# Kernel tuning notes

Measured on AMD Instinct MI355X. Metric: run time of the kernel, lower is better.

## Reference

```python
import jax, jax.numpy as jnp
import numpy as np

NUM_HEADS = 12


def setup_inputs() -> dict:
    key = jax.random.key(0)
    k1, k2, k3 = jax.random.split(key, 3)
    B, S, D = 8, 1024, 768
    x = jax.random.normal(k1, (B, S, D), dtype=jnp.float32)
    # Linear weights, torch convention [out_features, in_features], small init
    w_qkv = jax.random.normal(k2, (3 * D, D), dtype=jnp.float32) * 0.02
    b_qkv = jnp.zeros((3 * D,), dtype=jnp.float32)
    w_proj = jax.random.normal(k3, (D, D), dtype=jnp.float32) * 0.02
    b_proj = jnp.zeros((D,), dtype=jnp.float32)
    return {"x": x, "w_qkv": w_qkv, "b_qkv": b_qkv, "w_proj": w_proj, "b_proj": b_proj}


def reference(x, w_qkv, b_qkv, w_proj, b_proj):
    B, S, D = x.shape
    H = NUM_HEADS
    hd = D // H
    qkv = x @ w_qkv.T + b_qkv                      # [B, S, 3D]
    qkv = qkv.reshape(B, S, 3, H, hd).transpose(2, 0, 3, 1, 4)  # [3, B, H, S, hd]
    q, k, v = qkv[0], qkv[1], qkv[2]
    # NOTE: source computes self.scale but never applies it -> unscaled QK^T
    weights = jnp.einsum('bhqd,bhkd->bhqk', q, k)  # [B, H, S, S]
    attn = jax.nn.softmax(weights, axis=-1)        # dropout = 0 (eval)
    out = jnp.einsum('bhqk,bhkd->bhqd', attn, v)   # [B, H, S, hd]
    out = out.transpose(0, 2, 1, 3).reshape(B, S, D)
    return out @ w_proj.T + b_proj
```

## Files before the change

kernel.cpp:

```cpp
#include <hip/hip_runtime.h>


typedef short bf16x8 __attribute__((ext_vector_type(8)));
typedef float f32x4  __attribute__((ext_vector_type(4)));

#define MFMA16(a, b, c) __builtin_amdgcn_mfma_f32_16x16x32_bf16((a), (b), (c), 0, 0, 0)

__device__ __forceinline__ unsigned short f2bf(float f) {
    union { float f; unsigned int u; } v; v.f = f;
    unsigned int u = v.u;
    return (unsigned short)((u + 0x7fffu + ((u >> 16) & 1u)) >> 16);
}

__device__ __forceinline__ unsigned int cvt2(float x, float y) {
#if __has_builtin(__builtin_amdgcn_cvt_pk_bf16_f32)
    auto v = __builtin_amdgcn_cvt_pk_bf16_f32(x, y);
    unsigned int b; __builtin_memcpy(&b, &v, 4); return b;
#else
    return (unsigned int)f2bf(x) | ((unsigned int)f2bf(y) << 16);
#endif
}

__device__ __forceinline__ void gl2lds16(const unsigned short* g, unsigned short* l) {
    __builtin_amdgcn_global_load_lds(
        (const unsigned int __attribute__((address_space(1)))*)g,
        (unsigned int __attribute__((address_space(3)))*)l,
        16, 0, 0);
}

__global__ void cvt_kernel(const float* __restrict__ src,
                           unsigned short* __restrict__ dst, int n4) {
    int i = blockIdx.x * blockDim.x + threadIdx.x;
    if (i >= n4) return;
    float4 v = ((const float4*)src)[i];
    ushort4 o;
    o.x = f2bf(v.x); o.y = f2bf(v.y); o.z = f2bf(v.z); o.w = f2bf(v.w);
    ((ushort4*)dst)[i] = o;
}

__global__ __launch_bounds__(256) void gemm_qkv(
    const unsigned short* __restrict__ A,
    const unsigned short* __restrict__ Bm,
    const float* __restrict__ bias,
    unsigned short* __restrict__ Qo,
    unsigned short* __restrict__ Ko,
    unsigned short* __restrict__ Vto) {
    const int K = 768;
    __shared__ __align__(16) unsigned short smem[8704];
    unsigned short* As = smem;
    unsigned short* Bs = smem + 4096;
    const int tid = threadIdx.x;
    const int wave = tid >> 6, lane = tid & 63;
    const int quad = lane >> 4, l16 = lane & 15;
    const int wm = (wave >> 1) * 64, wn = (wave & 1) * 64;
    const int tileM = blockIdx.x * 128, tileN = blockIdx.y * 128;

    f32x4 zero4 = {0.f, 0.f, 0.f, 0.f};
    f32x4 acc[4][4];
#pragma unroll
    for (int i = 0; i < 4; ++i)
#pragma unroll
        for (int j = 0; j < 4; ++j) acc[i][j] = zero4;

    const unsigned short* Ab = A + (size_t)tileM * K;
    const unsigned short* Bb = Bm + (size_t)tileN * K;

    for (int k0 = 0; k0 < K; k0 += 32) {
#pragma unroll
        for (int i = 0; i < 2; ++i) {
            int s = tid + (i << 8);
            int r = s >> 2, c = s & 3;
            gl2lds16(Ab + (size_t)r * K + k0 + c * 8, As + ((wave << 6) + (i << 8)) * 8);
            gl2lds16(Bb + (size_t)r * K + k0 + c * 8, Bs + ((wave << 6) + (i << 8)) * 8);
        }
        __syncthreads();
        bf16x8 af[4], bfr[4];
#pragma unroll
        for (int t = 0; t < 4; ++t) {
            af[t]  = *(const bf16x8*)(As + (wm + t * 16 + l16) * 32 + quad * 8);
            bfr[t] = *(const bf16x8*)(Bs + (wn + t * 16 + l16) * 32 + quad * 8);
        }
#pragma unroll
        for (int tm = 0; tm < 4; ++tm)
#pragma unroll
            for (int tn = 0; tn < 4; ++tn)
                acc[tm][tn] = MFMA16(af[tm], bfr[tn], acc[tm][tn]);
        __syncthreads();
    }

    const int t = blockIdx.y / 6;
    if (t < 2) {
        const float scale = (t == 0) ? 1.44269504f : 1.0f;
        unsigned short* dst = (t == 0) ? Qo : Ko;
#pragma unroll
        for (int tm = 0; tm < 4; ++tm) {
#pragma unroll
            for (int tn = 0; tn < 4; ++tn) {
                int n = tileN + wn + tn * 16 + l16;
                int rem = n - t * 768;
                int h = rem >> 6, d = rem & 63;
                float bv = bias[n];
#pragma unroll
                for (int r = 0; r < 4; ++r) {
                    int m = tileM + wm + tm * 16 + quad * 4 + r;
                    int b = m >> 10, s = m & 1023;
                    dst[((((size_t)b * 12 + h) << 10) + s) * 64 + d] =
                        f2bf((acc[tm][tn][r] + bv) * scale);
                }
            }
        }
    } else {
        const int b = tileM >> 10, srow = tileM & 1023;
#pragma unroll
        for (int h2 = 0; h2 < 2; ++h2) {
            __syncthreads();
            if ((wn >> 6) == h2) {
#pragma unroll
                for (int tn = 0; tn < 4; ++tn) {
                    int dl = tn * 16 + l16;
                    float bv = bias[tileN + wn + dl];
#pragma unroll
                    for (int tm = 0; tm < 4; ++tm) {
                        int mb = wm + tm * 16 + quad * 4;
                        uint2 pk;
                        pk.x = cvt2(acc[tm][tn][0] + bv, acc[tm][tn][1] + bv);
                        pk.y = cvt2(acc[tm][tn][2] + bv, acc[tm][tn][3] + bv);
                        *(uint2*)(smem + dl * 136 + mb) = pk;
                    }
                }
            }
            __syncthreads();
#pragma unroll
            for (int pass = 0; pass < 4; ++pass) {
                int dl = pass * 16 + (tid >> 4), soff = (tid & 15) * 8;
                bf16x8 row = *(const bf16x8*)(smem + dl * 136 + soff);
                int rem = tileN + h2 * 64 + dl - 1536;
                int h = rem >> 6, d = rem & 63;
                *(bf16x8*)(Vto + (((size_t)b * 12 + h) * 64 + d) * 1024 + srow + soff) = row;
            }
        }
    }
}

__global__ __launch_bounds__(256) void attn_kernel(
    const unsigned short* __restrict__ Q,
    const unsigned short* __restrict__ Kg,
    const unsigned short* __restrict__ Vt,
    unsigned short* __restrict__ O) {
    __shared__ __align__(16) unsigned short Qs[2][128 * 32];
    __shared__ __align__(16) unsigned short Ks[2][64 * 32];
    __shared__ __align__(16) unsigned short Vs[2][64 * 32];
    __shared__ __align__(16) unsigned short Ps[128 * 64];

    const int tid = threadIdx.x;
    const int wave = tid >> 6, lane = tid & 63;
    const int quad = lane >> 4, l16 = lane & 15;
    const int s4 = l16 & 3;
    const int qt = blockIdx.x;
    const int bh = blockIdx.y;
    const int b = bh / 12, h = bh - b * 12;

    const unsigned short* Qb = Q  + ((size_t)bh * 1024 + qt * 128) * 64;
    const unsigned short* Kb = Kg + (size_t)bh * 1024 * 64;
    const unsigned short* Vb = Vt + (size_t)bh * 64 * 1024;

#pragma unroll
    for (int half = 0; half < 2; ++half)
#pragma unroll
        for (int i = 0; i < 2; ++i) {
            int s = tid + (i << 8);
            int r = s >> 2, c = s & 3;
            gl2lds16(Qb + r * 64 + half * 32 + c * 8,
                     Qs[half] + ((wave << 6) + (i << 8)) * 8);
        }

    f32x4 zero4 = {0.f, 0.f, 0.f, 0.f};
    f32x4 oacc[2][4], osum[2];
#pragma unroll
    for (int tm = 0; tm < 2; ++tm) {
        osum[tm] = zero4;
#pragma unroll
        for (int tv = 0; tv < 4; ++tv) oacc[tm][tv] = zero4;
    }
    const short one_bf = (short)0x3F80;
    const bf16x8 onef = {one_bf, one_bf, one_bf, one_bf,
                         one_bf, one_bf, one_bf, one_bf};

    for (int kv0 = 0; kv0 < 1024; kv0 += 64) {
        {
            int r = tid >> 2, c = tid & 3;
#pragma unroll
            for (int half = 0; half < 2; ++half) {
                gl2lds16(Kb + (size_t)(kv0 + r) * 64 + half * 32 + c * 8,
                         Ks[half] + (wave << 6) * 8);
                gl2lds16(Vb + (size_t)r * 1024 + kv0 + half * 32 + c * 8,
                         Vs[half] + (wave << 6) * 8);
            }
        }
        __syncthreads();

        f32x4 st[4][2];
#pragma unroll
        for (int tk = 0; tk < 4; ++tk)
#pragma unroll
            for (int tq = 0; tq < 2; ++tq) st[tk][tq] = zero4;
#pragma unroll
        for (int ks = 0; ks < 2; ++ks) {
            bf16x8 kf[4], qf[2];
#pragma unroll
            for (int tk = 0; tk < 4; ++tk)
                kf[tk] = *(const bf16x8*)(Ks[ks] + (tk * 16 + l16) * 32 + quad * 8);
#pragma unroll
            for (int tq = 0; tq < 2; ++tq)
                qf[tq] = *(const bf16x8*)(Qs[ks] + (wave * 32 + tq * 16 + l16) * 32 + quad * 8);
#pragma unroll
            for (int tk = 0; tk < 4; ++tk)
#pragma unroll
                for (int tq = 0; tq < 2; ++tq)
                    st[tk][tq] = MFMA16(kf[tk], qf[tq], st[tk][tq]);
        }

#pragma unroll
        for (int tq = 0; tq < 2; ++tq) {
            unsigned short* prp = Ps + (wave * 32 + tq * 16 + l16) * 64 + quad * 4;
#pragma unroll
            for (int tk = 0; tk < 4; ++tk) {
                float e0 = __builtin_amdgcn_exp2f(st[tk][tq][0]);
                float e1 = __builtin_amdgcn_exp2f(st[tk][tq][1]);
                float e2 = __builtin_amdgcn_exp2f(st[tk][tq][2]);
                float e3 = __builtin_amdgcn_exp2f(st[tk][tq][3]);
                uint2 pk;
                pk.x = cvt2(e0, e1);
                pk.y = cvt2(e2, e3);
                *(uint2*)(prp + ((tk ^ s4) << 4)) = pk;
            }
        }

#pragma unroll
        for (int ks2 = 0; ks2 < 2; ++ks2) {
            bf16x8 ap[2], bv[4];
            int colswz = ((ks2 << 5) + (quad << 3)) ^ (s4 << 4);
#pragma unroll
            for (int tm = 0; tm < 2; ++tm)
                ap[tm] = *(const bf16x8*)(Ps + (wave * 32 + tm * 16 + l16) * 64 + colswz);
#pragma unroll
            for (int tv = 0; tv < 4; ++tv)
                bv[tv] = *(const bf16x8*)(Vs[ks2] + (tv * 16 + l16) * 32 + quad * 8);
#pragma unroll
            for (int tm = 0; tm < 2; ++tm) {
#pragma unroll
                for (int tv = 0; tv < 4; ++tv)
                    oacc[tm][tv] = MFMA16(ap[tm], bv[tv], oacc[tm][tv]);
                osum[tm] = MFMA16(ap[tm], onef, osum[tm]);
            }
        }
        __syncthreads();
    }

#pragma unroll
    for (int tm = 0; tm < 2; ++tm) {
        f32x4 inv;
#pragma unroll
        for (int r = 0; r < 4; ++r) inv[r] = 1.0f / osum[tm][r];
#pragma unroll
        for (int tv = 0; tv < 4; ++tv)
#pragma unroll
            for (int r = 0; r < 4; ++r) {
                int srow = qt * 128 + wave * 32 + tm * 16 + quad * 4 + r;
                int col = h * 64 + tv * 16 + l16;
                O[((size_t)b * 1024 + srow) * 768 + col] = f2bf(oacc[tm][tv][r] * inv[r]);
            }
    }
}

__global__ __launch_bounds__(256) void gemm_proj(
    const unsigned short* __restrict__ A,
    const unsigned short* __restrict__ Bm,
    const float* __restrict__ bias,
    float* __restrict__ out) {
    const int K = 768;
    __shared__ __align__(16) unsigned short As[128 * 32];
    __shared__ __align__(16) unsigned short Bs[128 * 32];
    const int tid = threadIdx.x;
    const int wave = tid >> 6, lane = tid & 63;
    const int quad = lane >> 4, l16 = lane & 15;
    const int wm = (wave >> 1) * 64, wn = (wave & 1) * 64;
    const int tileM = blockIdx.x * 128, tileN = blockIdx.y * 128;

    f32x4 zero4 = {0.f, 0.f, 0.f, 0.f};
    f32x4 acc[4][4];
#pragma unroll
    for (int i = 0; i < 4; ++i)
#pragma unroll
        for (int j = 0; j < 4; ++j) acc[i][j] = zero4;

    const unsigned short* Ab = A + (size_t)tileM * K;
    const unsigned short* Bb = Bm + (size_t)tileN * K;

    for (int k0 = 0; k0 < K; k0 += 32) {
#pragma unroll
        for (int i = 0; i < 2; ++i) {
            int s = tid + (i << 8);
            int r = s >> 2, c = s & 3;
            gl2lds16(Ab + (size_t)r * K + k0 + c * 8, As + ((wave << 6) + (i << 8)) * 8);
            gl2lds16(Bb + (size_t)r * K + k0 + c * 8, Bs + ((wave << 6) + (i << 8)) * 8);
        }
        __syncthreads();
        bf16x8 af[4], bfr[4];
#pragma unroll
        for (int t = 0; t < 4; ++t) {
            af[t]  = *(const bf16x8*)(As + (wm + t * 16 + l16) * 32 + quad * 8);
            bfr[t] = *(const bf16x8*)(Bs + (wn + t * 16 + l16) * 32 + quad * 8);
        }
#pragma unroll
        for (int tm = 0; tm < 4; ++tm)
#pragma unroll
            for (int tn = 0; tn < 4; ++tn)
                acc[tm][tn] = MFMA16(af[tm], bfr[tn], acc[tm][tn]);
        __syncthreads();
    }

#pragma unroll
    for (int tm = 0; tm < 4; ++tm) {
#pragma unroll
        for (int tn = 0; tn < 4; ++tn) {
            int n = tileN + wn + tn * 16 + l16;
            float bv = bias[n];
#pragma unroll
            for (int r = 0; r < 4; ++r) {
                int m = tileM + wm + tm * 16 + quad * 4 + r;
                out[(size_t)m * 768 + n] = acc[tm][tn][r] + bv;
            }
        }
    }
}

extern "C" void kernel_launch(void* const* d_in, const int* in_sizes, int n_in,
                              void* d_out, int out_size, void* d_ws, size_t ws_size,
                              hipStream_t stream) {
    (void)in_sizes; (void)n_in; (void)out_size; (void)ws_size;
    const float* x      = (const float*)d_in[0];
    const float* w_qkv  = (const float*)d_in[1];
    const float* b_qkv  = (const float*)d_in[2];
    const float* w_proj = (const float*)d_in[3];
    const float* b_proj = (const float*)d_in[4];
    float* out = (float*)d_out;

    char* ws = (char*)d_ws;
    unsigned short* xb     = (unsigned short*)(ws + 0);
    unsigned short* wqkvb  = (unsigned short*)(ws + 12582912);
    unsigned short* wprojb = (unsigned short*)(ws + 16121856);
    unsigned short* Qw     = (unsigned short*)(ws + 17301504);
    unsigned short* Kw     = (unsigned short*)(ws + 29884416);
    unsigned short* Vtw    = (unsigned short*)(ws + 42467328);

    cvt_kernel<<<(1572864 + 255) / 256, 256, 0, stream>>>(x, xb, 1572864);
    cvt_kernel<<<(442368 + 255) / 256, 256, 0, stream>>>(w_qkv, wqkvb, 442368);
    cvt_kernel<<<(147456 + 255) / 256, 256, 0, stream>>>(w_proj, wprojb, 147456);

    gemm_qkv<<<dim3(64, 18), 256, 0, stream>>>(xb, wqkvb, b_qkv, Qw, Kw, Vtw);
    attn_kernel<<<dim3(8, 96), 256, 0, stream>>>(Qw, Kw, Vtw, xb);
    gemm_proj<<<dim3(64, 6), 256, 0, stream>>>(xb, wprojb, b_proj, out);
}
```

Baseline: 210.3 us.

## Merge conversion kernels, deepen GEMM K-step, restructure attention Q/K layout and row sums

Merges the three fp32-to-bf16 conversion launches into one kernel. Doubles the K step per barrier in both GEMMs, loading two 32-wide slabs per iteration to halve synchronisation. Q and K are now written in a row-major [B,S,D] layout with coalesced stores instead of per-head scattered stores. The attention kernel keeps Q fragments in registers, accumulates softmax row sums with scalar adds and shuffles instead of an extra MFMA against ones, and aliases its LDS buffers. The trade-offs are more LDS per block, which may reduce occupancy, and strided per-head K/Q loads in attention.

```diff
diff --git a/kernel.cpp b/kernel.cpp
--- a/kernel.cpp
+++ b/kernel.cpp
@@ -28,14 +28,21 @@
         16, 0, 0);
 }
 
-__global__ void cvt_kernel(const float* __restrict__ src,
-                           unsigned short* __restrict__ dst, int n4) {
-    int i = blockIdx.x * blockDim.x + threadIdx.x;
-    if (i >= n4) return;
-    float4 v = ((const float4*)src)[i];
+__global__ void cvt3_kernel(const float* __restrict__ x,
+                            const float* __restrict__ wq,
+                            const float* __restrict__ wp,
+                            unsigned short* __restrict__ xb,
+                            unsigned short* __restrict__ wqb,
+                            unsigned short* __restrict__ wpb) {
+    int i = blockIdx.x * 256 + threadIdx.x;
+    const float* s; unsigned short* d; int off;
+    if (i < 1572864)      { s = x;  d = xb;  off = i; }
+    else if (i < 2015232) { s = wq; d = wqb; off = i - 1572864; }
+    else                  { s = wp; d = wpb; off = i - 2015232; }
+    float4 v = ((const float4*)s)[off];
     ushort4 o;
     o.x = f2bf(v.x); o.y = f2bf(v.y); o.z = f2bf(v.z); o.w = f2bf(v.w);
-    ((ushort4*)dst)[i] = o;
+    ((ushort4*)d)[off] = o;
 }
 
 __global__ __launch_bounds__(256) void gemm_qkv(
@@ -46,9 +53,9 @@
     unsigned short* __restrict__ Ko,
     unsigned short* __restrict__ Vto) {
     const int K = 768;
-    __shared__ __align__(16) unsigned short smem[8704];
-    unsigned short* As = smem;
-    unsigned short* Bs = smem + 4096;
+    __shared__ __align__(16) unsigned short smem[16384];
+    unsigned short* Asv[2] = { smem, smem + 4096 };
+    unsigned short* Bsv[2] = { smem + 8192, smem + 12288 };
     const int tid = threadIdx.x;
     const int wave = tid >> 6, lane = tid & 63;
     const int quad = lane >> 4, l16 = lane & 15;
@@ -65,26 +72,34 @@
     const unsigned short* Ab = A + (size_t)tileM * K;
     const unsigned short* Bb = Bm + (size_t)tileN * K;
 
-    for (int k0 = 0; k0 < K; k0 += 32) {
+    for (int k0 = 0; k0 < K; k0 += 64) {
 #pragma unroll
         for (int i = 0; i < 2; ++i) {
             int s = tid + (i << 8);
             int r = s >> 2, c = s & 3;
-            gl2lds16(Ab + (size_t)r * K + k0 + c * 8, As + ((wave << 6) + (i << 8)) * 8);
-            gl2lds16(Bb + (size_t)r * K + k0 + c * 8, Bs + ((wave << 6) + (i << 8)) * 8);
-        }
-        __syncthreads();
-        bf16x8 af[4], bfr[4];
-#pragma unroll
-        for (int t = 0; t < 4; ++t) {
-            af[t]  = *(const bf16x8*)(As + (wm + t * 16 + l16) * 32 + quad * 8);
-            bfr[t] = *(const bf16x8*)(Bs + (wn + t * 16 + l16) * 32 + quad * 8);
-        }
-#pragma unroll
-        for (int tm = 0; tm < 4; ++tm)
-#pragma unroll
-            for (int tn = 0; tn < 4; ++tn)
-                acc[tm][tn] = MFMA16(af[tm], bfr[tn], acc[tm][tn]);
+            const unsigned short* ga = Ab + (size_t)r * K + k0 + c * 8;
+            const unsigned short* gb = Bb + (size_t)r * K + k0 + c * 8;
+            int dst = ((wave << 6) + (i << 8)) * 8;
+            gl2lds16(ga,      Asv[0] + dst);
+            gl2lds16(ga + 32, Asv[1] + dst);
+            gl2lds16(gb,      Bsv[0] + dst);
+            gl2lds16(gb + 32, Bsv[1] + dst);
+        }
+        __syncthreads();
+#pragma unroll
+        for (int ks = 0; ks < 2; ++ks) {
+            bf16x8 af[4], bfr[4];
+#pragma unroll
+            for (int t = 0; t < 4; ++t) {
+                af[t]  = *(const bf16x8*)(Asv[ks] + (wm + t * 16 + l16) * 32 + quad * 8);
+                bfr[t] = *(const bf16x8*)(Bsv[ks] + (wn + t * 16 + l16) * 32 + quad * 8);
+            }
+#pragma unroll
+            for (int tm = 0; tm < 4; ++tm)
+#pragma unroll
+                for (int tn = 0; tn < 4; ++tn)
+                    acc[tm][tn] = MFMA16(af[tm], bfr[tn], acc[tm][tn]);
+        }
         __syncthreads();
     }
 
@@ -92,20 +107,17 @@
     if (t < 2) {
         const float scale = (t == 0) ? 1.44269504f : 1.0f;
         unsigned short* dst = (t == 0) ? Qo : Ko;
+        const int nb = tileN - t * 768 + wn;
 #pragma unroll
         for (int tm = 0; tm < 4; ++tm) {
 #pragma unroll
             for (int tn = 0; tn < 4; ++tn) {
-                int n = tileN + wn + tn * 16 + l16;
-                int rem = n - t * 768;
-                int h = rem >> 6, d = rem & 63;
-                float bv = bias[n];
+                int nl = nb + tn * 16 + l16;
+                float bv = bias[tileN + wn + tn * 16 + l16];
 #pragma unroll
                 for (int r = 0; r < 4; ++r) {
                     int m = tileM + wm + tm * 16 + quad * 4 + r;
-                    int b = m >> 10, s = m & 1023;
-                    dst[((((size_t)b * 12 + h) << 10) + s) * 64 + d] =
-                        f2bf((acc[tm][tn][r] + bv) * scale);
+                    dst[(size_t)m * 768 + nl] = f2bf((acc[tm][tn][r] + bv) * scale);
                 }
             }
         }
@@ -147,10 +159,11 @@
     const unsigned short* __restrict__ Kg,
     const unsigned short* __restrict__ Vt,
     unsigned short* __restrict__ O) {
-    __shared__ __align__(16) unsigned short Qs[2][128 * 32];
-    __shared__ __align__(16) unsigned short Ks[2][64 * 32];
-    __shared__ __align__(16) unsigned short Vs[2][64 * 32];
-    __shared__ __align__(16) unsigned short Ps[128 * 64];
+    __shared__ __align__(16) unsigned short smem[16384];
+    unsigned short* Ps  = smem;
+    unsigned short* Qsv[2] = { smem, smem + 4096 };
+    unsigned short* Ksv[2] = { smem + 8192,  smem + 10240 };
+    unsigned short* Vsv[2] = { smem + 12288, smem + 14336 };
 
     const int tid = threadIdx.x;
     const int wave = tid >> 6, lane = tid & 63;
@@ -160,42 +173,46 @@
     const int bh = blockIdx.y;
     const int b = bh / 12, h = bh - b * 12;
 
-    const unsigned short* Qb = Q  + ((size_t)bh * 1024 + qt * 128) * 64;
-    const unsigned short* Kb = Kg + (size_t)bh * 1024 * 64;
+    const unsigned short* Qb = Q  + ((size_t)b * 1024 + qt * 128) * 768 + h * 64;
+    const unsigned short* Kb = Kg + (size_t)b * 1024 * 768 + h * 64;
     const unsigned short* Vb = Vt + (size_t)bh * 64 * 1024;
 
 #pragma unroll
-    for (int half = 0; half < 2; ++half)
-#pragma unroll
-        for (int i = 0; i < 2; ++i) {
-            int s = tid + (i << 8);
-            int r = s >> 2, c = s & 3;
-            gl2lds16(Qb + r * 64 + half * 32 + c * 8,
-                     Qs[half] + ((wave << 6) + (i << 8)) * 8);
-        }
+    for (int i = 0; i < 2; ++i) {
+        int s = tid + (i << 8);
+        int r = s >> 2, c = s & 3;
+        const unsigned short* gq = Qb + (size_t)r * 768 + c * 8;
+        int dst = ((wave << 6) + (i << 8)) * 8;
+        gl2lds16(gq,      Qsv[0] + dst);
+        gl2lds16(gq + 32, Qsv[1] + dst);
+    }
+    __syncthreads();
+    bf16x8 qf[2][2];
+#pragma unroll
+    for (int ks = 0; ks < 2; ++ks)
+#pragma unroll
+        for (int tq = 0; tq < 2; ++tq)
+            qf[ks][tq] = *(const bf16x8*)(Qsv[ks] + (wave * 32 + tq * 16 + l16) * 32 + quad * 8);
+    __syncthreads();
 
     f32x4 zero4 = {0.f, 0.f, 0.f, 0.f};
-    f32x4 oacc[2][4], osum[2];
-#pragma unroll
-    for (int tm = 0; tm < 2; ++tm) {
-        osum[tm] = zero4;
+    f32x4 oacc[2][4];
+    float rsum[2] = {0.f, 0.f};
+#pragma unroll
+    for (int tm = 0; tm < 2; ++tm)
 #pragma unroll
         for (int tv = 0; tv < 4; ++tv) oacc[tm][tv] = zero4;
-    }
-    const short one_bf = (short)0x3F80;
-    const bf16x8 onef = {one_bf, one_bf, one_bf, one_bf,
-                         one_bf, one_bf, one_bf, one_bf};
 
     for (int kv0 = 0; kv0 < 1024; kv0 += 64) {
         {
             int r = tid >> 2, c = tid & 3;
-#pragma unroll
-            for (int half = 0; half < 2; ++half) {
-                gl2lds16(Kb + (size_t)(kv0 + r) * 64 + half * 32 + c * 8,
-                         Ks[half] + (wave << 6) * 8);
-                gl2lds16(Vb + (size_t)r * 1024 + kv0 + half * 32 + c * 8,
-                         Vs[half] + (wave << 6) * 8);
-            }
+            const unsigned short* gk = Kb + (size_t)(kv0 + r) * 768 + c * 8;
+            const unsigned short* gv = Vb + (size_t)r * 1024 + kv0 + c * 8;
+            int dst = (wave << 6) * 8;
+            gl2lds16(gk,      Ksv[0] + dst);
+            gl2lds16(gk + 32, Ksv[1] + dst);
+            gl2lds16(gv,      Vsv[0] + dst);
+            gl2lds16(gv + 32, Vsv[1] + dst);
         }
         __syncthreads();
 
@@ -206,18 +223,15 @@
             for (int tq = 0; tq < 2; ++tq) st[tk][tq] = zero4;
 #pragma unroll
         for (int ks = 0; ks < 2; ++ks) {
-            bf16x8 kf[4], qf[2];
+            bf16x8 kf[4];
 #pragma unroll
             for (int tk = 0; tk < 4; ++tk)
-                kf[tk] = *(const bf16x8*)(Ks[ks] + (tk * 16 + l16) * 32 + quad * 8);
-#pragma unroll
-            for (int tq = 0; tq < 2; ++tq)
-                qf[tq] = *(const bf16x8*)(Qs[ks] + (wave * 32 + tq * 16 + l16) * 32 + quad * 8);
+                kf[tk] = *(const bf16x8*)(Ksv[ks] + (tk * 16 + l16) * 32 + quad * 8);
 #pragma unroll
             for (int tk = 0; tk < 4; ++tk)
 #pragma unroll
                 for (int tq = 0; tq < 2; ++tq)
-                    st[tk][tq] = MFMA16(kf[tk], qf[tq], st[tk][tq]);
+                    st[tk][tq] = MFMA16(kf[tk], qf[ks][tq], st[tk][tq]);
         }
 
 #pragma unroll
@@ -229,6 +243,7 @@
                 float e1 = __builtin_amdgcn_exp2f(st[tk][tq][1]);
                 float e2 = __builtin_amdgcn_exp2f(st[tk][tq][2]);
                 float e3 = __builtin_amdgcn_exp2f(st[tk][tq][3]);
+                rsum[tq] += (e0 + e1) + (e2 + e3);
                 uint2 pk;
                 pk.x = cvt2(e0, e1);
                 pk.y = cvt2(e2, e3);
@@ -245,23 +260,34 @@
                 ap[tm] = *(const bf16x8*)(Ps + (wave * 32 + tm * 16 + l16) * 64 + colswz);
 #pragma unroll
             for (int tv = 0; tv < 4; ++tv)
-                bv[tv] = *(const bf16x8*)(Vs[ks2] + (tv * 16 + l16) * 32 + quad * 8);
-#pragma unroll
-            for (int tm = 0; tm < 2; ++tm) {
+                bv[tv] = *(const bf16x8*)(Vsv[ks2] + (tv * 16 + l16) * 32 + quad * 8);
+#pragma unroll
+            for (int tm = 0; tm < 2; ++tm)
 #pragma unroll
                 for (int tv = 0; tv < 4; ++tv)
                     oacc[tm][tv] = MFMA16(ap[tm], bv[tv], oacc[tm][tv]);
-                osum[tm] = MFMA16(ap[tm], onef, osum[tm]);
-            }
-        }
-        __syncthreads();
-    }
+        }
+        __syncthreads();
+    }
+
+#pragma unroll
+    for (int tq = 0; tq < 2; ++tq) {
+        rsum[tq] += __shfl_xor(rsum[tq], 16, 64);
+        rsum[tq] += __shfl_xor(rsum[tq], 32, 64);
+    }
+    float* sums = (float*)smem;
+    if (quad == 0) {
+        sums[wave * 32 + l16]      = rsum[0];
+        sums[wave * 32 + 16 + l16] = rsum[1];
+    }
+    __syncthreads();
 
 #pragma unroll
     for (int tm = 0; tm < 2; ++tm) {
         f32x4 inv;
 #pragma unroll
-        for (int r = 0; r < 4; ++r) inv[r] = 1.0f / osum[tm][r];
+        for (int r = 0; r < 4; ++r)
+            inv[r] = 1.0f / sums[wave * 32 + tm * 16 + quad * 4 + r];
 #pragma unroll
         for (int tv = 0; tv < 4; ++tv)
 #pragma unroll
@@ -279,8 +305,9 @@
     const float* __restrict__ bias,
     float* __restrict__ out) {
     const int K = 768;
-    __shared__ __align__(16) unsigned short As[128 * 32];
-    __shared__ __align__(16) unsigned short Bs[128 * 32];
+    __shared__ __align__(16) unsigned short smem[16384];
+    unsigned short* Asv[2] = { smem, smem + 4096 };
+    unsigned short* Bsv[2] = { smem + 8192, smem + 12288 };
     const int tid = threadIdx.x;
     const int wave = tid >> 6, lane = tid & 63;
     const int quad = lane >> 4, l16 = lane & 15;
@@ -297,26 +324,34 @@
     const unsigned short* Ab = A + (size_t)tileM * K;
     const unsigned short* Bb = Bm + (size_t)tileN * K;
 
-    for (int k0 = 0; k0 < K; k0 += 32) {
+    for (int k0 = 0; k0 < K; k0 += 64) {
 #pragma unroll
         for (int i = 0; i < 2; ++i) {
             int s = tid + (i << 8);
             int r = s >> 2, c = s & 3;
-            gl2lds16(Ab + (size_t)r * K + k0 + c * 8, As + ((wave << 6) + (i << 8)) * 8);
-            gl2lds16(Bb + (size_t)r * K + k0 + c * 8, Bs + ((wave << 6) + (i << 8)) * 8);
-        }
-        __syncthreads();
-        bf16x8 af[4], bfr[4];
-#pragma unroll
-        for (int t = 0; t < 4; ++t) {
-            af[t]  = *(const bf16x8*)(As + (wm + t * 16 + l16) * 32 + quad * 8);
-            bfr[t] = *(const bf16x8*)(Bs + (wn + t * 16 + l16) * 32 + quad * 8);
-        }
-#pragma unroll
-        for (int tm = 0; tm < 4; ++tm)
-#pragma unroll
-            for (int tn = 0; tn < 4; ++tn)
-                acc[tm][tn] = MFMA16(af[tm], bfr[tn], acc[tm][tn]);
+            const unsigned short* ga = Ab + (size_t)r * K + k0 + c * 8;
+            const unsigned short* gb = Bb + (size_t)r * K + k0 + c * 8;
+            int dst = ((wave << 6) + (i << 8)) * 8;
+            gl2lds16(ga,      Asv[0] + dst);
+            gl2lds16(ga + 32, Asv[1] + dst);
+            gl2lds16(gb,      Bsv[0] + dst);
+            gl2lds16(gb + 32, Bsv[1] + dst);
+        }
+        __syncthreads();
+#pragma unroll
+        for (int ks = 0; ks < 2; ++ks) {
+            bf16x8 af[4], bfr[4];
+#pragma unroll
+            for (int t = 0; t < 4; ++t) {
+                af[t]  = *(const bf16x8*)(Asv[ks] + (wm + t * 16 + l16) * 32 + quad * 8);
+                bfr[t] = *(const bf16x8*)(Bsv[ks] + (wn + t * 16 + l16) * 32 + quad * 8);
+            }
+#pragma unroll
+            for (int tm = 0; tm < 4; ++tm)
+#pragma unroll
+                for (int tn = 0; tn < 4; ++tn)
+                    acc[tm][tn] = MFMA16(af[tm], bfr[tn], acc[tm][tn]);
+        }
         __syncthreads();
     }
 
@@ -354,10 +389,7 @@
     unsigned short* Kw     = (unsigned short*)(ws + 29884416);
     unsigned short* Vtw    = (unsigned short*)(ws + 42467328);
 
-    cvt_kernel<<<(1572864 + 255) / 256, 256, 0, stream>>>(x, xb, 1572864);
-    cvt_kernel<<<(442368 + 255) / 256, 256, 0, stream>>>(w_qkv, wqkvb, 442368);
-    cvt_kernel<<<(147456 + 255) / 256, 256, 0, stream>>>(w_proj, wprojb, 147456);
-
+    cvt3_kernel<<<8448, 256, 0, stream>>>(x, w_qkv, w_proj, xb, wqkvb, wprojb);
     gemm_qkv<<<dim3(64, 18), 256, 0, stream>>>(xb, wqkvb, b_qkv, Qw, Kw, Vtw);
     attn_kernel<<<dim3(8, 96), 256, 0, stream>>>(Qw, Kw, Vtw, xb);
     gemm_proj<<<dim3(64, 6), 256, 0, stream>>>(xb, wprojb, b_proj, out);
```

Result: slower. 224.1 us (+6.6%).
